# Kernel tuning notes

Hardware: AMD Instinct MI355X
Metric: run time of the kernel (lower is better)

## Reference

```python
import jax, jax.numpy as jnp
import numpy as np

B, N, D, E, H = 16, 1024, 1024, 4, 16


def setup_inputs() -> dict:
    key = jax.random.key(0)
    k1, k2, k3, k4 = jax.random.split(key, 4)
    return {
        "input_tokens": jax.random.normal(k1, (B, N, D), dtype=jnp.float32),
        "expert_mask": jax.random.randint(k2, (B, N), 0, E, dtype=jnp.int32),
        "qkv_w": jax.random.normal(k3, (3 * D, D), dtype=jnp.float32) * 0.02,
        "proj_w": jax.random.normal(k4, (D, D), dtype=jnp.float32) * 0.02,
        "proj_b": jnp.zeros((D,), dtype=jnp.float32),
    }


def reference(input_tokens, expert_mask, qkv_w, proj_w, proj_b):
    b, n, d = input_tokens.shape
    hd = d // H
    scale = 1.0 / np.sqrt(hd).astype(np.float32)
    # nested expert e uses first d_e = D / 2^(E-1-e) features (expert E-1 = full dim)
    d_tok = d // (2 ** (E - 1 - expert_mask))                     # [B, N]
    feat_mask = (jnp.arange(d)[None, None, :] < d_tok[..., None]).astype(input_tokens.dtype)  # [B, N, D]
    # NestedLinearExpand: slice input features per token (== mask), full 3D output
    x_in = input_tokens * feat_mask
    qkv = jnp.einsum('bnd,fd->bnf', x_in, qkv_w).reshape(b, n, 3, H, hd)
    q, k, v = jnp.moveaxis(qkv, 2, 0)                             # each [B, N, H, hd]
    q = q.transpose(0, 2, 1, 3)                                   # [B, H, N, hd]
    k = k.transpose(0, 2, 1, 3)
    v = v.transpose(0, 2, 1, 3)
    scores = jnp.einsum('bhqd,bhkd->bhqk', q, k) * scale          # [B, H, N, N]
    attn = jax.nn.softmax(scores, axis=-1)
    x = jnp.einsum('bhqk,bhkd->bhqd', attn, v)                    # [B, H, N, hd]
    x = x.transpose(0, 2, 1, 3).reshape(b, n, d)
    # NestedLinearContract: full-dim matmul, only first d_e outputs kept per token
    y = jnp.einsum('bnd,fd->bnf', x, proj_w) + proj_b
    return y * feat_mask
```

## Files before the change

### kernel.cpp

```cpp
#include <hip/hip_runtime.h>
#include <hip/hip_bf16.h>


typedef __bf16 bf16_t;
typedef __bf16 bf16x8 __attribute__((ext_vector_type(8)));
typedef __bf16 bf16x4 __attribute__((ext_vector_type(4)));
typedef float f32x4 __attribute__((ext_vector_type(4)));
typedef float f32x16 __attribute__((ext_vector_type(16)));
typedef int i32x4 __attribute__((ext_vector_type(4)));

typedef __attribute__((address_space(1))) void gvoid;
typedef __attribute__((address_space(3))) void lvoid;

#define MFMA16(a, b, c) __builtin_amdgcn_mfma_f32_16x16x32_bf16((a), (b), (c), 0, 0, 0)
#define MFMA32(a, b, c) __builtin_amdgcn_mfma_f32_32x32x16_bf16((a), (b), (c), 0, 0, 0)
#define GLOAD_LDS16(gsrc, ldst) \
  __builtin_amdgcn_global_load_lds((gvoid*)(gsrc), (lvoid*)(ldst), 16, 0, 0)

#define QSCALE 0.18033688f

__device__ __forceinline__ unsigned cvtpk(float lo, float hi) {
  unsigned r;
  asm("v_cvt_pk_bf16_f32 %0, %1, %2" : "=v"(r) : "v"(lo), "v"(hi));
  return r;
}
__device__ __forceinline__ void pl32swap(unsigned& x, unsigned& y) {
  asm("v_permlane32_swap_b32 %0, %1" : "+v"(x), "+v"(y));
}

__global__ __launch_bounds__(256) void sort_batch(
    const int* __restrict__ em, int* __restrict__ perm, int* __restrict__ ems) {
  __shared__ int cnt[4], base[4], cur[4];
  const int b = blockIdx.x, t = threadIdx.x;
  if (t < 4) cnt[t] = 0;
  __syncthreads();
  int e[4];
#pragma unroll
  for (int i = 0; i < 4; ++i) {
    e[i] = em[b * 1024 + t * 4 + i];
    atomicAdd(&cnt[e[i]], 1);
  }
  __syncthreads();
  if (t == 0) {
    base[0] = 0; base[1] = cnt[0];
    base[2] = cnt[0] + cnt[1]; base[3] = cnt[0] + cnt[1] + cnt[2];
    cur[0] = cur[1] = cur[2] = cur[3] = 0;
  }
  __syncthreads();
#pragma unroll
  for (int i = 0; i < 4; ++i) {
    const int pos = base[e[i]] + atomicAdd(&cur[e[i]], 1);
    perm[b * 1024 + pos] = t * 4 + i;
    ems[b * 1024 + pos] = e[i];
  }
}

__global__ __launch_bounds__(256) void prep_tokens(
    const float* __restrict__ x, const int* __restrict__ perm,
    const int* __restrict__ ems, bf16_t* __restrict__ xq) {
  const int prow = blockIdx.x;
  const int orig = (prow & ~1023) + perm[prow];
  const int dt = 128 << ems[prow];
  const int d = threadIdx.x * 4;
  float4 v = ((const float4*)(x + (size_t)orig * 1024))[threadIdx.x];
  const bool keep = d < dt;
  bf16x4 o;
  o[0] = (bf16_t)(keep ? v.x : 0.f);
  o[1] = (bf16_t)(keep ? v.y : 0.f);
  o[2] = (bf16_t)(keep ? v.z : 0.f);
  o[3] = (bf16_t)(keep ? v.w : 0.f);
  *((bf16x4*)(xq + (size_t)prow * 1024 + d)) = o;
}

__global__ __launch_bounds__(256) void conv_w(
    const float* __restrict__ s, bf16_t* __restrict__ dvec) {
  const int i = blockIdx.x * 256 + threadIdx.x;
  float4 v = ((const float4*)s)[i];
  bf16x4 o;
  o[0] = (bf16_t)v.x; o[1] = (bf16_t)v.y; o[2] = (bf16_t)v.z; o[3] = (bf16_t)v.w;
  ((bf16x4*)dvec)[i] = o;
}

template <int EPI>
__global__ __launch_bounds__(512, 2) void gemm256(
    const bf16_t* __restrict__ A, const bf16_t* __restrict__ Bw, int K,
    const int* __restrict__ perm, const int* __restrict__ ems,
    bf16_t* __restrict__ qo, bf16_t* __restrict__ ko, bf16_t* __restrict__ vto,
    float* __restrict__ yout, const float* __restrict__ bias) {
  __shared__ bf16_t lds[2][32768];
  const int tid = threadIdx.x;
  const int lane = tid & 63, w = tid >> 6;
  const int wm = w >> 2, wn = w & 3;
  const int g = lane >> 4, c16 = lane & 15;

  const int bid = blockIdx.x;
  const int rowbase = (bid & 63) * 256;
  const int colbase = (bid >> 6) * 256;

  const int dtmax = 128 << ems[rowbase + 255];

  if constexpr (EPI == 1) {
    if (colbase >= dtmax) {
      const float4 z = make_float4(0.f, 0.f, 0.f, 0.f);
#pragma unroll
      for (int i = 0; i < 32; ++i) {
        const int idx = i * 512 + tid;
        const int r = idx >> 6, c4 = idx & 63;
        const int orow = ((rowbase + r) & ~1023) + perm[rowbase + r];
        ((float4*)(yout + (size_t)orow * 1024 + colbase))[c4] = z;
      }
      return;
    }
  }

  const int NT = (EPI == 0) ? (dtmax >> 6) : (K >> 6);

  const int trow = tid >> 3;
  const int scol = (((tid & 7) ^ (trow & 7)) << 3);
  const bf16_t* pa = A + (size_t)(rowbase + trow) * K + scol;
  const bf16_t* pb = Bw + (size_t)(colbase + trow) * K + scol;

#define STAGE(j, koff, dst)                                       \
  GLOAD_LDS16(((j) < 4 ? pa + (size_t)((j) * 64) * K              \
                       : pb + (size_t)(((j) - 4) * 64) * K) +     \
                  (koff),                                         \
              (dst) + ((j) * 512 + tid) * 8)

#define LDFRAG(base, R, kk)            \
  (*(const bf16x8*)((base) + (size_t)(R) * 64 + \
                    (((((kk) << 2) + g) ^ (c16 & 7)) << 3)))

  f32x4 acc[8][4] = {};

#pragma unroll
  for (int j = 0; j < 8; ++j) STAGE(j, 0, (bf16_t*)lds[0]);
  asm volatile("s_waitcnt vmcnt(0)" ::: "memory");
  __builtin_amdgcn_s_barrier();

  for (int t = 0; t < NT; ++t) {
    const bf16_t* Lb = lds[t & 1];
    const bf16_t* LbB = Lb + 16384;
    const bool pf = (t + 1) < NT;

    if (pf) {
      bf16_t* Sd = (bf16_t*)lds[(t + 1) & 1];
      const int koff = (t + 1) << 6;
#pragma unroll
      for (int j = 0; j < 8; ++j) STAGE(j, koff, Sd);
    }

    bf16x8 af[4][2], af2[4][2], b0[2][2], b1[2][2];
#pragma unroll
    for (int mi = 0; mi < 4; ++mi)
#pragma unroll
      for (int kk = 0; kk < 2; ++kk)
        af[mi][kk] = LDFRAG(Lb, wm * 128 + mi * 16 + c16, kk);
#pragma unroll
    for (int ni = 0; ni < 2; ++ni)
#pragma unroll
      for (int kk = 0; kk < 2; ++kk)
        b0[ni][kk] = LDFRAG(LbB, wn * 64 + ni * 16 + c16, kk);
#pragma unroll
    for (int mi = 0; mi < 4; ++mi)
#pragma unroll
      for (int ni = 0; ni < 2; ++ni)
#pragma unroll
        for (int kk = 0; kk < 2; ++kk)
          acc[mi][ni] = MFMA16(af[mi][kk], b0[ni][kk], acc[mi][ni]);

#pragma unroll
    for (int ni = 0; ni < 2; ++ni)
#pragma unroll
      for (int kk = 0; kk < 2; ++kk)
        b1[ni][kk] = LDFRAG(LbB, wn * 64 + (ni + 2) * 16 + c16, kk);
#pragma unroll
    for (int mi = 0; mi < 4; ++mi)
#pragma unroll
      for (int ni = 0; ni < 2; ++ni)
#pragma unroll
        for (int kk = 0; kk < 2; ++kk)
          acc[mi][ni + 2] = MFMA16(af[mi][kk], b1[ni][kk], acc[mi][ni + 2]);

#pragma unroll
    for (int mi = 0; mi < 4; ++mi)
#pragma unroll
      for (int kk = 0; kk < 2; ++kk)
        af2[mi][kk] = LDFRAG(Lb, wm * 128 + (mi + 4) * 16 + c16, kk);
#pragma unroll
    for (int mi = 0; mi < 4; ++mi)
#pragma unroll
      for (int ni = 0; ni < 2; ++ni)
#pragma unroll
        for (int kk = 0; kk < 2; ++kk)
          acc[mi + 4][ni] = MFMA16(af2[mi][kk], b0[ni][kk], acc[mi + 4][ni]);

#pragma unroll
    for (int mi = 0; mi < 4; ++mi)
#pragma unroll
      for (int ni = 0; ni < 2; ++ni)
#pragma unroll
        for (int kk = 0; kk < 2; ++kk)
          acc[mi + 4][ni + 2] = MFMA16(af2[mi][kk], b1[ni][kk], acc[mi + 4][ni + 2]);

    if (pf) asm volatile("s_waitcnt vmcnt(0)" ::: "memory");
    __builtin_amdgcn_s_barrier();
  }

  char* epi = (char*)lds;
  if constexpr (EPI == 0) {
    const int s = colbase >> 10;
    const float qs = (s == 0) ? QSCALE : 1.0f;
    if (s < 2) {
#pragma unroll
      for (int mi = 0; mi < 8; ++mi)
#pragma unroll
        for (int ni = 0; ni < 4; ++ni)
#pragma unroll
          for (int j = 0; j < 4; ++j) {
            const int r = wm * 128 + mi * 16 + g * 4 + j;
            const int c = wn * 64 + ni * 16 + c16;
            *(bf16_t*)(epi + r * 512 + 2 * (c ^ (g << 4))) =
                (bf16_t)(acc[mi][ni][j] * qs);
          }
      __builtin_amdgcn_s_barrier();
      bf16_t* const dstbase = (s == 0) ? qo : ko;
#pragma unroll
      for (int it = 0; it < 16; ++it) {
        const int flat = it * 512 + tid;
        const int r = flat >> 5, c0 = (flat & 31) * 8;
        const int gr = (r >> 2) & 3;
        bf16x8 v = *(const bf16x8*)(epi + r * 512 + 2 * (c0 ^ (gr << 4)));
        const int prow = rowbase + r;
        const int bb = prow >> 10, n = prow & 1023;
        const int f = colbase + c0;
        const int h = (f >> 6) & 15, e = f & 63;
        const size_t bh = (size_t)(bb * 16 + h);
        *(bf16x8*)(dstbase + (bh * 1024 + n) * 64 + e) = v;
      }
    } else {
#pragma unroll
      for (int mi = 0; mi < 8; ++mi)
#pragma unroll
        for (int ni = 0; ni < 4; ++ni)
#pragma unroll
          for (int j = 0; j < 4; ++j) {
            const int r = wm * 128 + mi * 16 + g * 4 + j;
            const int c = wn * 64 + ni * 16 + c16;
            *(bf16_t*)(epi + c * 512 + 2 * (r ^ ((c16 >> 2) << 4))) =
                (bf16_t)acc[mi][ni][j];
          }
      __builtin_amdgcn_s_barrier();
      const int bb = rowbase >> 10;
      const int nb = rowbase & 1023;
#pragma unroll
      for (int it = 0; it < 16; ++it) {
        const int flat = it * 512 + tid;
        const int c = flat >> 5, r0 = (flat & 31) * 8;
        const int cc = (c >> 2) & 3;
        bf16x8 v = *(const bf16x8*)(epi + c * 512 + 2 * (r0 ^ (cc << 4)));
        const int f = colbase + c;
        const int h = (f >> 6) & 15, e = f & 63;
        const size_t bh = (size_t)(bb * 16 + h);
        *(bf16x8*)(vto + (bh * 64 + e) * 1024 + nb + r0) = v;
      }
    }
  } else {
#pragma unroll
    for (int p = 0; p < 2; ++p) {
      if (p) __builtin_amdgcn_s_barrier();
      if (wm == p) {
#pragma unroll
        for (int mi = 0; mi < 8; ++mi)
#pragma unroll
          for (int ni = 0; ni < 4; ++ni)
#pragma unroll
            for (int j = 0; j < 4; ++j) {
              const int rl = mi * 16 + g * 4 + j;
              const int c = wn * 64 + ni * 16 + c16;
              *(float*)(epi + rl * 1024 + 4 * (c ^ (g << 4))) = acc[mi][ni][j];
            }
      }
      __builtin_amdgcn_s_barrier();
#pragma unroll
      for (int it = 0; it < 16; ++it) {
        const int flat = it * 512 + tid;
        const int rl = flat >> 6, c0 = (flat & 63) * 4;
        const int gr = (rl >> 2) & 3;
        float4 v = *(const float4*)(epi + rl * 1024 + 4 * (c0 ^ (gr << 4)));
        const int pr = rowbase + p * 128 + rl;
        const int orow = (pr & ~1023) + perm[pr];
        const int dt = 128 << ems[pr];
        const int col = colbase + c0;
        const float4 bia = *(const float4*)(bias + col);
        const bool keep = col < dt;
        float4 o;
        o.x = keep ? v.x + bia.x : 0.f;
        o.y = keep ? v.y + bia.y : 0.f;
        o.z = keep ? v.z + bia.z : 0.f;
        o.w = keep ? v.w + bia.w : 0.f;
        *(float4*)(yout + (size_t)orow * 1024 + col) = o;
      }
    }
  }
#undef STAGE
#undef LDFRAG
}

__global__ __launch_bounds__(512, 2) void attn256(
    const bf16_t* __restrict__ Q, const bf16_t* __restrict__ Kb,
    const bf16_t* __restrict__ VT, bf16_t* __restrict__ X) {
  __shared__ bf16_t Klds[2][4096];
  __shared__ bf16_t Vlds[2][4096];
  const int tid = threadIdx.x;
  const int w = tid >> 6, lane = tid & 63;
  const int k32 = lane & 31, q5 = lane >> 5;
  const int bh = blockIdx.y;
  const int qbase = blockIdx.x * 256 + w * 32;

  const bf16_t* Qbh = Q + (size_t)bh * 65536;
  const bf16_t* Kbh = Kb + (size_t)bh * 65536;
  const bf16_t* Vbh = VT + (size_t)bh * 65536;

  const int trow = tid >> 3;
  const int tslot = (tid & 7) ^ (trow & 7);
  const bf16_t* kg = Kbh + (size_t)trow * 64 + tslot * 8;
  const bf16_t* vg = Vbh + (size_t)trow * 1024 + tslot * 8;

  bf16x8 qf[4];
#pragma unroll
  for (int kc = 0; kc < 4; ++kc)
    qf[kc] = *(const bf16x8*)(Qbh + (size_t)(qbase + k32) * 64 + kc * 16 + q5 * 8);
  asm volatile("" ::"v"(qf[0]), "v"(qf[1]), "v"(qf[2]), "v"(qf[3]));

  const int rbase = k32 * 128 + q5 * 16;
  const int rswz = (k32 & 7) << 4;

  f32x16 O0 = {}, O1 = {};
  float m = -3.0e38f, lsum = 0.f;

  GLOAD_LDS16(kg, (bf16_t*)Klds[0] + tid * 8);
  GLOAD_LDS16(vg, (bf16_t*)Vlds[0] + tid * 8);

  for (int step = 0; step < 16; ++step) {
    const int buf = step & 1;
    if (step < 15) {
      GLOAD_LDS16(kg + (step + 1) * 4096, (bf16_t*)Klds[buf ^ 1] + tid * 8);
      GLOAD_LDS16(vg + (step + 1) * 64, (bf16_t*)Vlds[buf ^ 1] + tid * 8);
      asm volatile("s_waitcnt vmcnt(2)" ::: "memory");
    } else {
      asm volatile("s_waitcnt vmcnt(0)" ::: "memory");
    }
    __builtin_amdgcn_s_barrier();

    const char* Kl = (const char*)Klds[buf];
    const char* Vl = (const char*)Vlds[buf];

    f32x16 S0 = {}, S1 = {};
#pragma unroll
    for (int kc = 0; kc < 4; ++kc) {
      const int off = (rbase + kc * 32) ^ rswz;
      bf16x8 kf0 = *(const bf16x8*)(Kl + off);
      bf16x8 kf1 = *(const bf16x8*)(Kl + off + 4096);
      S0 = MFMA32(kf0, qf[kc], S0);
      S1 = MFMA32(kf1, qf[kc], S1);
    }

    float pm = fmaxf(S0[0], S1[0]);
#pragma unroll
    for (int r = 1; r < 16; ++r) pm = fmaxf(pm, fmaxf(S0[r], S1[r]));
    pm = fmaxf(pm, __shfl_xor(pm, 32));
    if (__any(pm > m + 8.f)) {
      const float mnew = fmaxf(m, pm);
      const float corr = __builtin_amdgcn_exp2f(m - mnew);
      m = mnew;
      lsum *= corr;
      const int ci = __builtin_bit_cast(int, corr);
#pragma unroll
      for (int r = 0; r < 16; ++r) {
        const int qsel = (r & 3) + 8 * (r >> 2) + 4 * q5;
        const float cr = __builtin_bit_cast(
            float, __builtin_amdgcn_ds_bpermute(qsel << 2, ci));
        O0[r] *= cr;
        O1[r] *= cr;
      }
    }
    float ps = 0.f;
#pragma unroll
    for (int r = 0; r < 16; ++r) {
      float p = __builtin_amdgcn_exp2f(S0[r] - m);
      ps += p; S0[r] = p;
      p = __builtin_amdgcn_exp2f(S1[r] - m);
      ps += p; S1[r] = p;
    }
    lsum += ps;

#define MAKE_PA(PV, B0, PA)                            \
  {                                                    \
    unsigned a_ = cvtpk(PV[B0 + 0], PV[B0 + 1]);       \
    unsigned b_ = cvtpk(PV[B0 + 2], PV[B0 + 3]);       \
    unsigned c_ = cvtpk(PV[B0 + 4], PV[B0 + 5]);       \
    unsigned d_ = cvtpk(PV[B0 + 6], PV[B0 + 7]);       \
    pl32swap(a_, c_);                                  \
    pl32swap(b_, d_);                                  \
    i32x4 wv_;                                         \
    wv_[0] = a_; wv_[1] = b_; wv_[2] = c_; wv_[3] = d_; \
    PA = __builtin_bit_cast(bf16x8, wv_);              \
  }
#define PV_STEP(PV, B0, KS)                                       \
  {                                                               \
    bf16x8 pa;                                                    \
    MAKE_PA(PV, B0, pa);                                          \
    const int voff = (rbase + (KS) * 32) ^ rswz;                  \
    bf16x8 vf0 = *(const bf16x8*)(Vl + voff);                     \
    bf16x8 vf1 = *(const bf16x8*)(Vl + voff + 4096);              \
    O0 = MFMA32(pa, vf0, O0);                                     \
    O1 = MFMA32(pa, vf1, O1);                                     \
  }
    PV_STEP(S0, 0, 0)
    PV_STEP(S0, 8, 1)
    PV_STEP(S1, 0, 2)
    PV_STEP(S1, 8, 3)

    __builtin_amdgcn_s_barrier();
  }

  lsum += __shfl_xor(lsum, 32);
  const float rinv = 1.f / lsum;
  const int ri = __builtin_bit_cast(int, rinv);
  const int bb = bh >> 4, h = bh & 15;
  bf16_t* Xb = X + (size_t)bb * 1024 * 1024 + h * 64;
#pragma unroll
  for (int r = 0; r < 16; ++r) {
    const int qsel = (r & 3) + 8 * (r >> 2) + 4 * q5;
    const float rv = __builtin_bit_cast(
        float, __builtin_amdgcn_ds_bpermute(qsel << 2, ri));
    const size_t rowoff = (size_t)(qbase + qsel) * 1024;
    Xb[rowoff + k32] = (bf16_t)(O0[r] * rv);
    Xb[rowoff + 32 + k32] = (bf16_t)(O1[r] * rv);
  }
}

extern "C" void kernel_launch(void* const* d_in, const int* in_sizes, int n_in,
                              void* d_out, int out_size, void* d_ws,
                              size_t ws_size, hipStream_t stream) {
  const float* x = (const float*)d_in[0];
  const int* em = (const int*)d_in[1];
  const float* qkvw = (const float*)d_in[2];
  const float* projw = (const float*)d_in[3];
  const float* projb = (const float*)d_in[4];
  float* out = (float*)d_out;

  char* ws = (char*)d_ws;
  size_t off = 0;
  bf16_t* xin = (bf16_t*)(ws + off); off += (size_t)16384 * 1024 * 2;
  bf16_t* wq  = (bf16_t*)(ws + off); off += (size_t)3072 * 1024 * 2;
  bf16_t* wp  = (bf16_t*)(ws + off); off += (size_t)1024 * 1024 * 2;
  bf16_t* Qb  = (bf16_t*)(ws + off); off += (size_t)256 * 1024 * 64 * 2;
  bf16_t* Kb  = (bf16_t*)(ws + off); off += (size_t)256 * 1024 * 64 * 2;
  bf16_t* VTb = (bf16_t*)(ws + off); off += (size_t)256 * 64 * 1024 * 2;
  int* perm   = (int*)(ws + off); off += 16384 * 4;
  int* ems    = (int*)(ws + off); off += 16384 * 4;

  sort_batch<<<16, 256, 0, stream>>>(em, perm, ems);

  prep_tokens<<<16384, 256, 0, stream>>>(x, perm, ems, xin);
  conv_w<<<3072, 256, 0, stream>>>(qkvw, wq);
  conv_w<<<1024, 256, 0, stream>>>(projw, wp);

  gemm256<0><<<768, 512, 0, stream>>>(
      xin, wq, 1024, perm, ems, Qb, Kb, VTb, nullptr, nullptr);

  attn256<<<dim3(4, 256), 512, 0, stream>>>(Qb, Kb, VTb, xin);

  gemm256<1><<<256, 512, 0, stream>>>(
      xin, wp, 1024, perm, ems, nullptr, nullptr, nullptr, out, projb);
}
```

Baseline: 271.9 us.

## Double attention KV tile size, stage output via LDS, reorder grid

The attention kernel now stages 128 keys per pipeline step instead of 64, processing two 64-key halves per barrier pair. This halves the number of barriers and waits. The output is written through a swizzled LDS buffer so each row goes to global memory as coalesced 16-byte stores instead of scattered 2-byte stores. The grid is transposed so consecutive blocks belong to different heads. The cost is doubled LDS use per block, which may limit occupancy at two blocks per CU.

New measurement: 265.3 us. -2.4%, faster.

```diff
diff --git a/kernel.cpp b/kernel.cpp
--- a/kernel.cpp
+++ b/kernel.cpp
@@ -309,22 +309,34 @@
 __global__ __launch_bounds__(512, 2) void attn256(
     const bf16_t* __restrict__ Q, const bf16_t* __restrict__ Kb,
     const bf16_t* __restrict__ VT, bf16_t* __restrict__ X) {
-  __shared__ bf16_t Klds[2][4096];
-  __shared__ bf16_t Vlds[2][4096];
+  __shared__ bf16_t Klds[2][8192];
+  __shared__ bf16_t Vlds[2][8192];
   const int tid = threadIdx.x;
   const int w = tid >> 6, lane = tid & 63;
   const int k32 = lane & 31, q5 = lane >> 5;
-  const int bh = blockIdx.y;
-  const int qbase = blockIdx.x * 256 + w * 32;
+  const int bh = blockIdx.x;
+  const int qbase0 = blockIdx.y * 256;
+  const int qbase = qbase0 + w * 32;
 
   const bf16_t* Qbh = Q + (size_t)bh * 65536;
   const bf16_t* Kbh = Kb + (size_t)bh * 65536;
   const bf16_t* Vbh = VT + (size_t)bh * 65536;
 
-  const int trow = tid >> 3;
-  const int tslot = (tid & 7) ^ (trow & 7);
-  const bf16_t* kg = Kbh + (size_t)trow * 64 + tslot * 8;
-  const bf16_t* vg = Vbh + (size_t)trow * 1024 + tslot * 8;
+  const int ktrow = tid >> 3;
+  const int ktslot = (tid & 7) ^ (ktrow & 7);
+  const bf16_t* kg = Kbh + (size_t)ktrow * 64 + ktslot * 8;
+  const int vtrow = tid >> 4;
+  const int vtslot = (tid & 15) ^ (vtrow & 15);
+  const bf16_t* vg = Vbh + (size_t)vtrow * 1024 + vtslot * 8;
+
+#define STAGE_KV(b, kt)                                              \
+  {                                                                  \
+    GLOAD_LDS16(kg + (size_t)(kt) * 64, (bf16_t*)Klds[b] + tid * 8); \
+    GLOAD_LDS16(kg + (size_t)(kt) * 64 + 4096,                      \
+                (bf16_t*)Klds[b] + 4096 + tid * 8);                  \
+    GLOAD_LDS16(vg + (kt), (bf16_t*)Vlds[b] + tid * 8);              \
+    GLOAD_LDS16(vg + (kt) + 32768, (bf16_t*)Vlds[b] + 4096 + tid * 8); \
+  }
 
   bf16x8 qf[4];
 #pragma unroll
@@ -332,67 +344,68 @@
     qf[kc] = *(const bf16x8*)(Qbh + (size_t)(qbase + k32) * 64 + kc * 16 + q5 * 8);
   asm volatile("" ::"v"(qf[0]), "v"(qf[1]), "v"(qf[2]), "v"(qf[3]));
 
-  const int rbase = k32 * 128 + q5 * 16;
-  const int rswz = (k32 & 7) << 4;
+  const int rswz8 = (k32 & 7) << 4;
+  const int rswz16 = (k32 & 15) << 4;
 
   f32x16 O0 = {}, O1 = {};
   float m = -3.0e38f, lsum = 0.f;
 
-  GLOAD_LDS16(kg, (bf16_t*)Klds[0] + tid * 8);
-  GLOAD_LDS16(vg, (bf16_t*)Vlds[0] + tid * 8);
-
-  for (int step = 0; step < 16; ++step) {
+  STAGE_KV(0, 0);
+
+  for (int step = 0; step < 8; ++step) {
     const int buf = step & 1;
-    if (step < 15) {
-      GLOAD_LDS16(kg + (step + 1) * 4096, (bf16_t*)Klds[buf ^ 1] + tid * 8);
-      GLOAD_LDS16(vg + (step + 1) * 64, (bf16_t*)Vlds[buf ^ 1] + tid * 8);
-      asm volatile("s_waitcnt vmcnt(2)" ::: "memory");
+    if (step < 7) {
+      STAGE_KV(buf ^ 1, (step + 1) * 128);
+      asm volatile("s_waitcnt vmcnt(4)" ::: "memory");
     } else {
       asm volatile("s_waitcnt vmcnt(0)" ::: "memory");
     }
     __builtin_amdgcn_s_barrier();
 
-    const char* Kl = (const char*)Klds[buf];
     const char* Vl = (const char*)Vlds[buf];
 
-    f32x16 S0 = {}, S1 = {};
-#pragma unroll
-    for (int kc = 0; kc < 4; ++kc) {
-      const int off = (rbase + kc * 32) ^ rswz;
-      bf16x8 kf0 = *(const bf16x8*)(Kl + off);
-      bf16x8 kf1 = *(const bf16x8*)(Kl + off + 4096);
-      S0 = MFMA32(kf0, qf[kc], S0);
-      S1 = MFMA32(kf1, qf[kc], S1);
-    }
-
-    float pm = fmaxf(S0[0], S1[0]);
-#pragma unroll
-    for (int r = 1; r < 16; ++r) pm = fmaxf(pm, fmaxf(S0[r], S1[r]));
-    pm = fmaxf(pm, __shfl_xor(pm, 32));
-    if (__any(pm > m + 8.f)) {
-      const float mnew = fmaxf(m, pm);
-      const float corr = __builtin_amdgcn_exp2f(m - mnew);
-      m = mnew;
-      lsum *= corr;
-      const int ci = __builtin_bit_cast(int, corr);
+#pragma unroll
+    for (int h = 0; h < 2; ++h) {
+      const char* Kl = (const char*)Klds[buf] + h * 8192;
+
+      f32x16 S0 = {}, S1 = {};
+#pragma unroll
+      for (int kc = 0; kc < 4; ++kc) {
+        const int off = k32 * 128 + ((q5 * 16 + kc * 32) ^ rswz8);
+        bf16x8 kf0 = *(const bf16x8*)(Kl + off);
+        bf16x8 kf1 = *(const bf16x8*)(Kl + off + 4096);
+        S0 = MFMA32(kf0, qf[kc], S0);
+        S1 = MFMA32(kf1, qf[kc], S1);
+      }
+
+      float pm = fmaxf(S0[0], S1[0]);
+#pragma unroll
+      for (int r = 1; r < 16; ++r) pm = fmaxf(fmaxf(S0[r], S1[r]), pm);
+      pm = fmaxf(pm, __shfl_xor(pm, 32));
+      if (__any(pm > m + 8.f)) {
+        const float mnew = fmaxf(m, pm);
+        const float corr = __builtin_amdgcn_exp2f(m - mnew);
+        m = mnew;
+        lsum *= corr;
+        const int ci = __builtin_bit_cast(int, corr);
+#pragma unroll
+        for (int r = 0; r < 16; ++r) {
+          const int qsel = (r & 3) + 8 * (r >> 2) + 4 * q5;
+          const float cr = __builtin_bit_cast(
+              float, __builtin_amdgcn_ds_bpermute(qsel << 2, ci));
+          O0[r] *= cr;
+          O1[r] *= cr;
+        }
+      }
+      float ps = 0.f;
 #pragma unroll
       for (int r = 0; r < 16; ++r) {
-        const int qsel = (r & 3) + 8 * (r >> 2) + 4 * q5;
-        const float cr = __builtin_bit_cast(
-            float, __builtin_amdgcn_ds_bpermute(qsel << 2, ci));
-        O0[r] *= cr;
-        O1[r] *= cr;
-      }
-    }
-    float ps = 0.f;
-#pragma unroll
-    for (int r = 0; r < 16; ++r) {
-      float p = __builtin_amdgcn_exp2f(S0[r] - m);
-      ps += p; S0[r] = p;
-      p = __builtin_amdgcn_exp2f(S1[r] - m);
-      ps += p; S1[r] = p;
-    }
-    lsum += ps;
+        float p = __builtin_amdgcn_exp2f(S0[r] - m);
+        ps += p; S0[r] = p;
+        p = __builtin_amdgcn_exp2f(S1[r] - m);
+        ps += p; S1[r] = p;
+      }
+      lsum += ps;
 
 #define MAKE_PA(PV, B0, PA)                            \
   {                                                    \
@@ -406,20 +419,21 @@
     wv_[0] = a_; wv_[1] = b_; wv_[2] = c_; wv_[3] = d_; \
     PA = __builtin_bit_cast(bf16x8, wv_);              \
   }
-#define PV_STEP(PV, B0, KS)                                       \
-  {                                                               \
-    bf16x8 pa;                                                    \
-    MAKE_PA(PV, B0, pa);                                          \
-    const int voff = (rbase + (KS) * 32) ^ rswz;                  \
-    bf16x8 vf0 = *(const bf16x8*)(Vl + voff);                     \
-    bf16x8 vf1 = *(const bf16x8*)(Vl + voff + 4096);              \
-    O0 = MFMA32(pa, vf0, O0);                                     \
-    O1 = MFMA32(pa, vf1, O1);                                     \
-  }
-    PV_STEP(S0, 0, 0)
-    PV_STEP(S0, 8, 1)
-    PV_STEP(S1, 0, 2)
-    PV_STEP(S1, 8, 3)
+#define PV_STEP(PV, B0, KS)                                         \
+  {                                                                 \
+    bf16x8 pa;                                                      \
+    MAKE_PA(PV, B0, pa);                                            \
+    const int voff = k32 * 256 + ((q5 * 16 + (KS) * 32) ^ rswz16);  \
+    bf16x8 vf0 = *(const bf16x8*)(Vl + voff);                       \
+    bf16x8 vf1 = *(const bf16x8*)(Vl + voff + 8192);                \
+    O0 = MFMA32(pa, vf0, O0);                                       \
+    O1 = MFMA32(pa, vf1, O1);                                       \
+  }
+      PV_STEP(S0, 0, h * 4 + 0)
+      PV_STEP(S0, 8, h * 4 + 1)
+      PV_STEP(S1, 0, h * 4 + 2)
+      PV_STEP(S1, 8, h * 4 + 3)
+    }
 
     __builtin_amdgcn_s_barrier();
   }
@@ -427,17 +441,30 @@
   lsum += __shfl_xor(lsum, 32);
   const float rinv = 1.f / lsum;
   const int ri = __builtin_bit_cast(int, rinv);
-  const int bb = bh >> 4, h = bh & 15;
-  bf16_t* Xb = X + (size_t)bb * 1024 * 1024 + h * 64;
+  char* Xs = (char*)Klds;
 #pragma unroll
   for (int r = 0; r < 16; ++r) {
     const int qsel = (r & 3) + 8 * (r >> 2) + 4 * q5;
     const float rv = __builtin_bit_cast(
         float, __builtin_amdgcn_ds_bpermute(qsel << 2, ri));
-    const size_t rowoff = (size_t)(qbase + qsel) * 1024;
-    Xb[rowoff + k32] = (bf16_t)(O0[r] * rv);
-    Xb[rowoff + 32 + k32] = (bf16_t)(O1[r] * rv);
-  }
+    const int row = w * 32 + qsel;
+    const int msk = (row & 7) << 4;
+    *(bf16_t*)(Xs + row * 128 + ((2 * k32) ^ msk)) = (bf16_t)(O0[r] * rv);
+    *(bf16_t*)(Xs + row * 128 + ((64 + 2 * k32) ^ msk)) = (bf16_t)(O1[r] * rv);
+  }
+  __builtin_amdgcn_s_barrier();
+  const int bb = bh >> 4, h = bh & 15;
+  bf16_t* Xb = X + (size_t)bb * 1024 * 1024 + h * 64;
+#pragma unroll
+  for (int it = 0; it < 4; ++it) {
+    const int flat = it * 512 + tid;
+    const int row = flat >> 3, ch = flat & 7;
+    bf16x8 v = *(const bf16x8*)(Xs + row * 128 + ((ch * 16) ^ ((row & 7) << 4)));
+    *(bf16x8*)(Xb + (size_t)(qbase0 + row) * 1024 + ch * 8) = v;
+  }
+#undef STAGE_KV
+#undef MAKE_PA
+#undef PV_STEP
 }
 
 extern "C" void kernel_launch(void* const* d_in, const int* in_sizes, int n_in,
@@ -470,7 +497,7 @@
   gemm256<0><<<768, 512, 0, stream>>>(
       xin, wq, 1024, perm, ems, Qb, Kb, VTb, nullptr, nullptr);
 
-  attn256<<<dim3(4, 256), 512, 0, stream>>>(Qb, Kb, VTb, xin);
+  attn256<<<dim3(256, 4), 512, 0, stream>>>(Qb, Kb, VTb, xin);
 
   gemm256<1><<<256, 512, 0, stream>>>(
       xin, wp, 1024, perm, ems, nullptr, nullptr, nullptr, out, projb);
```
